# Kernel tuning notes

Hardware: AMD Instinct MI355X
Metric: run time of the kernel (lower is better)

## Reference

```python
import jax, jax.numpy as jnp
import numpy as np

B, FDIM, H, E = 16384, 512, 256, 128  # batch, feature_dim, lstm hidden, scenario encoding


def setup_inputs() -> dict:
    key = jax.random.key(0)
    ks = jax.random.split(key, 24)
    p = lambda k, shape: (jax.random.normal(k, shape, jnp.float32) * 0.05)
    return {
        "base_timeline": jax.random.normal(ks[0], (B, FDIM), jnp.float32),
        "counterfactual_scenario": jax.random.normal(ks[1], (B, FDIM), jnp.float32),
        # scenario_encoder: Linear(512,256) -> ReLU -> Linear(256,128)
        "w_se1": p(ks[2], (256, FDIM)), "b_se1": p(ks[3], (256,)),
        "w_se2": p(ks[4], (E, 256)), "b_se2": p(ks[5], (E,)),
        # LSTM layer 0: input 128, hidden 256 (gate order i,f,g,o)
        "w_ih0": p(ks[6], (4 * H, E)), "w_hh0": p(ks[7], (4 * H, H)),
        "b_ih0": p(ks[8], (4 * H,)), "b_hh0": p(ks[9], (4 * H,)),
        # LSTM layer 1: input 256, hidden 256
        "w_ih1": p(ks[10], (4 * H, H)), "w_hh1": p(ks[11], (4 * H, H)),
        "b_ih1": p(ks[12], (4 * H,)), "b_hh1": p(ks[13], (4 * H,)),
        # outcome_modifier: Linear(384,256) -> ReLU -> Linear(256,512) -> Tanh
        "w_om1": p(ks[14], (256, H + E)), "b_om1": p(ks[15], (256,)),
        "w_om2": p(ks[16], (FDIM, 256)), "b_om2": p(ks[17], (FDIM,)),
        # probability_estimator: Linear(512,128) -> ReLU -> Linear(128,1) -> Sigmoid
        "w_pe1": p(ks[18], (E, FDIM)), "b_pe1": p(ks[19], (E,)),
        "w_pe2": p(ks[20], (1, E)), "b_pe2": p(ks[21], (1,)),
        "num_steps": 10,
    }


def _lstm_cell(x_pre, h, c, w_hh, b_hh):
    gates = x_pre + h @ w_hh.T + b_hh  # [B, 4H]
    i, f, g, o = jnp.split(gates, 4, axis=-1)
    c = jax.nn.sigmoid(f) * c + jax.nn.sigmoid(i) * jnp.tanh(g)
    h = jax.nn.sigmoid(o) * jnp.tanh(c)
    return h, c


def reference(base_timeline, counterfactual_scenario,
              w_se1, b_se1, w_se2, b_se2,
              w_ih0, w_hh0, b_ih0, b_hh0,
              w_ih1, w_hh1, b_ih1, b_hh1,
              w_om1, b_om1, w_om2, b_om2,
              w_pe1, b_pe1, w_pe2, b_pe2,
              num_steps):
    # scenario encoding [B, 128]
    s = jax.nn.relu(counterfactual_scenario @ w_se1.T + b_se1) @ w_se2.T + b_se2
    bsz = base_timeline.shape[0]
    h = w_hh0.shape[1]
    # LSTM layer-0 input is the same scenario encoding each step -> precompute
    x_pre0 = s @ w_ih0.T + b_ih0  # [B, 4H]

    def step(carry, _):
        cur, h0, c0, h1, c1 = carry
        h0, c0 = _lstm_cell(x_pre0, h0, c0, w_hh0, b_hh0)
        x1 = h0 @ w_ih1.T + b_ih1
        h1, c1 = _lstm_cell(x1, h1, c1, w_hh1, b_hh1)
        comb = jnp.concatenate([h1, s], axis=-1)  # [B, 384]
        mod = jnp.tanh(jax.nn.relu(comb @ w_om1.T + b_om1) @ w_om2.T + b_om2)
        nxt = cur + 0.1 * mod
        prob = jax.nn.sigmoid(jax.nn.relu(nxt @ w_pe1.T + b_pe1) @ w_pe2.T + b_pe2)
        return (nxt, h0, c0, h1, c1), (nxt, prob)

    z = jnp.zeros((bsz, h), base_timeline.dtype)
    (final, _, _, _, _), (states, probs) = jax.lax.scan(
        step, (base_timeline, z, z, z, z), None, length=num_steps)
    alternate_timeline = jnp.swapaxes(states, 0, 1)        # [B, num_steps, 512]
    timeline_probabilities = jnp.swapaxes(probs, 0, 1)     # [B, num_steps, 1]
    return alternate_timeline, timeline_probabilities, s, final
```

## Files before the change

### kernel.cpp

```cpp
#include <hip/hip_runtime.h>

typedef short bf16x8 __attribute__((ext_vector_type(8)));
typedef float f32x4 __attribute__((ext_vector_type(4)));

#define DEV __device__ __forceinline__

DEV short f2bf(float f) {
  union { float f; unsigned u; } v; v.f = f;
  unsigned r = v.u + 0x7FFFu + ((v.u >> 16) & 1u);
  return (short)(r >> 16);
}
DEV float bf2f(short s) {
  union { unsigned u; float f; } v; v.u = ((unsigned)(unsigned short)s) << 16;
  return v.f;
}
DEV float sigm(float x) { return 1.0f / (1.0f + __expf(-x)); }
DEV float tanh_(float x) {
  float a = fabsf(x);
  float e = __expf(-2.0f * a);
  float t = (1.0f - e) / (1.0f + e);
  return copysignf(t, x);
}

#define LDS_S    0
#define LDS_H0   16384
#define LDS_H1   49152
#define LDS_U    81920
#define LDS_NX   81920
#define LDS_PROB 147456
#define LDS_CF   16384
#define LDS_SZ   149504

#define OFF_SE1 0
#define OFF_SE2 131072
#define OFF_W0  163840
#define OFF_W1  557056
#define OFF_OM1 1081344
#define OFF_OM2 1179648
#define OFF_PE1 1310720

__global__ void prep_frag(const float* __restrict__ srcA, const float* __restrict__ srcB,
                          short* __restrict__ dst, int N, int K, int ksplit)
{
  const int e = blockIdx.x * 256 + threadIdx.x;
  if (e >= N * K) return;
  const int f = e >> 9;
  const int rix = e & 511;
  const int lane = rix >> 3, j = rix & 7;
  const int KK = K >> 5;
  const int ntile = f / KK, kk = f - ntile * KK;
  const int n = ntile * 16 + (lane & 15);
  const int k = kk * 32 + ((lane >> 4) << 3) + j;
  float v;
  if (k < ksplit) v = srcA[(size_t)n * ksplit + k];
  else            v = srcB[(size_t)n * (K - ksplit) + (k - ksplit)];
  dst[e] = f2bf(v);
}

template<int NT, int MT>
DEV void zacc(f32x4 (&acc)[NT][MT]) {
  #pragma unroll
  for (int n = 0; n < NT; ++n)
    #pragma unroll
    for (int m = 0; m < MT; ++m)
      acc[n][m] = (f32x4){0.f, 0.f, 0.f, 0.f};
}

template<int KK, int NT, int MT>
DEV void mm_tiles(const char* sm, int aBase0, int aStride0, int splitKB,
                  int aBase1, int aStride1,
                  const short* __restrict__ wf, int ntBase, int ntStride,
                  f32x4 (&acc)[NT][MT], int lane)
{
  const int l15 = lane & 15, l4 = lane >> 4;
  const short* wp = wf + lane * 8;
  bf16x8 b[2][NT];
  #pragma unroll
  for (int nt = 0; nt < NT; ++nt)
    b[0][nt] = *(const bf16x8*)(wp + (size_t)((ntBase + nt * ntStride) * KK) * 512);
  #pragma unroll
  for (int kk = 0; kk < KK; ++kk) {
    const int cb = kk & 1, nb = cb ^ 1;
    if (kk + 1 < KK) {
      #pragma unroll
      for (int nt = 0; nt < NT; ++nt)
        b[nb][nt] = *(const bf16x8*)(wp + (size_t)((ntBase + nt * ntStride) * KK + kk + 1) * 512);
    }
    const int kb = kk * 64 + l4 * 16;
    bf16x8 a[MT];
    #pragma unroll
    for (int m = 0; m < MT; ++m) {
      const int r = m * 16 + l15;
      int off;
      if (kb < splitKB) off = aBase0 + r * aStride0 + (kb ^ ((r & 7) << 4));
      else              off = aBase1 + r * aStride1 + ((kb - splitKB) ^ ((r & 7) << 4));
      a[m] = *(const bf16x8*)(sm + off);
    }
    #pragma unroll
    for (int nt = 0; nt < NT; ++nt)
      #pragma unroll
      for (int m = 0; m < MT; ++m)
        acc[nt][m] = __builtin_amdgcn_mfma_f32_16x16x32_bf16(a[m], b[cb][nt], acc[nt][m], 0, 0, 0);
  }
}

DEV void lstm_ew(f32x4 (&acc)[4][4], f32x4 bv, unsigned (&cpk)[8], unsigned (&hp)[16], int hoff)
{
  #pragma unroll
  for (int m = 0; m < 4; ++m)
    #pragma unroll
    for (int qh = 0; qh < 2; ++qh) {
      const int pi = m * 2 + qh;
      const unsigned oldc = cpk[pi];
      unsigned newc = 0, newh = 0;
      #pragma unroll
      for (int ql = 0; ql < 2; ++ql) {
        const int q = qh * 2 + ql;
        const float gi = acc[0][m][q] + bv[0];
        const float gf = acc[1][m][q] + bv[1];
        const float gg = acc[2][m][q] + bv[2];
        const float go = acc[3][m][q] + bv[3];
        const float cold = bf2f((short)((oldc >> (ql * 16)) & 0xFFFFu));
        const float c = sigm(gf) * cold + sigm(gi) * tanh_(gg);
        const float h = sigm(go) * tanh_(c);
        newc |= ((unsigned)(unsigned short)f2bf(c)) << (ql * 16);
        newh |= ((unsigned)(unsigned short)f2bf(h)) << (ql * 16);
      }
      cpk[pi] = newc;
      hp[hoff + pi] = newh;
    }
}

__global__ __launch_bounds__(512, 2) void atg_main(
    const float* __restrict__ base, const float* __restrict__ cf,
    const float* __restrict__ b_se1, const float* __restrict__ b_se2,
    const float* __restrict__ b_ih0, const float* __restrict__ b_hh0,
    const float* __restrict__ b_ih1, const float* __restrict__ b_hh1,
    const float* __restrict__ b_om1, const float* __restrict__ b_om2,
    const float* __restrict__ b_pe1, const float* __restrict__ w_pe2,
    const float* __restrict__ b_pe2,
    const short* __restrict__ wsb,
    float* __restrict__ outStates, float* __restrict__ probs,
    float* __restrict__ outS, float* __restrict__ outFinal, int nsteps)
{
  __shared__ __align__(16) char sm[LDS_SZ];
  const int tid = threadIdx.x;
  const int lane = tid & 63, wid = tid >> 6;
  const int l15 = lane & 15, l4 = lane >> 4;
  const int row0 = blockIdx.x * 64;

  float curv[64];
  #pragma unroll
  for (int nt = 0; nt < 4; ++nt)
    #pragma unroll
    for (int m = 0; m < 4; ++m)
      #pragma unroll
      for (int q = 0; q < 4; ++q)
        curv[nt * 16 + m * 4 + q] =
            base[(size_t)(row0 + m * 16 + l4 * 4 + q) * 512 + wid * 64 + nt * 16 + l15];

  {
    const int r = tid >> 3, ci = tid & 7;
    const float* src = cf + (size_t)(row0 + r) * 512;
    #pragma unroll
    for (int i = 0; i < 16; ++i) {
      const int c = ci * 4 + i * 32;
      const float4 v = *(const float4*)(src + c);
      short4 h; h.x = f2bf(v.x); h.y = f2bf(v.y); h.z = f2bf(v.z); h.w = f2bf(v.w);
      *(short4*)(sm + LDS_CF + r * 1024 + ((c * 2) ^ ((r & 7) << 4))) = h;
    }
  }
  __syncthreads();

  {
    f32x4 acc[2][4]; zacc(acc);
    mm_tiles<16, 2, 4>(sm, LDS_CF, 1024, 1 << 28, LDS_CF, 1024, wsb + OFF_SE1, wid * 2, 1, acc, lane);
    #pragma unroll
    for (int nt = 0; nt < 2; ++nt) {
      const int cc = wid * 32 + nt * 16 + l15;
      const float bv = b_se1[cc];
      #pragma unroll
      for (int m = 0; m < 4; ++m)
        #pragma unroll
        for (int q = 0; q < 4; ++q) {
          const int rr = m * 16 + l4 * 4 + q;
          const float u = fmaxf(acc[nt][m][q] + bv, 0.0f);
          *(short*)(sm + LDS_U + rr * 512 + ((cc * 2) ^ ((rr & 7) << 4))) = f2bf(u);
        }
    }
  }
  __syncthreads();

  {
    f32x4 acc[1][4]; zacc(acc);
    mm_tiles<8, 1, 4>(sm, LDS_U, 512, 1 << 28, LDS_U, 512, wsb + OFF_SE2, wid, 1, acc, lane);
    const int cc = wid * 16 + l15;
    const float bv = b_se2[cc];
    #pragma unroll
    for (int m = 0; m < 4; ++m)
      #pragma unroll
      for (int q = 0; q < 4; ++q) {
        const int rr = m * 16 + l4 * 4 + q;
        const float v = acc[0][m][q] + bv;
        __builtin_nontemporal_store(v, outS + (size_t)(row0 + rr) * 128 + cc);
        *(short*)(sm + LDS_S + rr * 256 + ((cc * 2) ^ ((rr & 7) << 4))) = f2bf(v);
      }
    #pragma unroll
    for (int i = 0; i < 8; ++i)
      *(f32x4*)(sm + LDS_H0 + tid * 128 + i * 16) = (f32x4){0.f, 0.f, 0.f, 0.f};
  }
  __syncthreads();

  f32x4 b0v[2], b1v[2];
  #pragma unroll
  for (int js = 0; js < 2; ++js) {
    f32x4 t0, t1;
    #pragma unroll
    for (int g = 0; g < 4; ++g) {
      const int c = g * 256 + wid * 32 + js * 16 + l15;
      t0[g] = b_ih0[c] + b_hh0[c];
      t1[g] = b_ih1[c] + b_hh1[c];
    }
    b0v[js] = t0; b1v[js] = t1;
  }

  unsigned c0a[8], c0b[8], c1a[8], c1b[8];
  #pragma unroll
  for (int i = 0; i < 8; ++i) { c0a[i] = 0u; c0b[i] = 0u; c1a[i] = 0u; c1b[i] = 0u; }

  for (int step = 0; step < nsteps; ++step) {
    unsigned hp[16];
    {
      f32x4 acc[4][4]; zacc(acc);
      mm_tiles<12, 4, 4>(sm, LDS_S, 256, 256, LDS_H0, 512, wsb + OFF_W0, wid * 2 + 0, 16, acc, lane);
      lstm_ew(acc, b0v[0], c0a, hp, 0);
    }
    {
      f32x4 acc[4][4]; zacc(acc);
      mm_tiles<12, 4, 4>(sm, LDS_S, 256, 256, LDS_H0, 512, wsb + OFF_W0, wid * 2 + 1, 16, acc, lane);
      lstm_ew(acc, b0v[1], c0b, hp, 8);
    }
    __syncthreads();
    #pragma unroll
    for (int js = 0; js < 2; ++js)
      #pragma unroll
      for (int m = 0; m < 4; ++m)
        #pragma unroll
        for (int q = 0; q < 4; ++q) {
          const int rr = m * 16 + l4 * 4 + q;
          const int cc = wid * 32 + js * 16 + l15;
          const unsigned v = hp[js * 8 + m * 2 + (q >> 1)] >> ((q & 1) * 16);
          *(short*)(sm + LDS_H0 + rr * 512 + ((cc * 2) ^ ((rr & 7) << 4))) = (short)v;
        }
    __syncthreads();
    {
      f32x4 acc[4][4]; zacc(acc);
      mm_tiles<16, 4, 4>(sm, LDS_H0, 512, 512, LDS_H1, 512, wsb + OFF_W1, wid * 2 + 0, 16, acc, lane);
      lstm_ew(acc, b1v[0], c1a, hp, 0);
    }
    {
      f32x4 acc[4][4]; zacc(acc);
      mm_tiles<16, 4, 4>(sm, LDS_H0, 512, 512, LDS_H1, 512, wsb + OFF_W1, wid * 2 + 1, 16, acc, lane);
      lstm_ew(acc, b1v[1], c1b, hp, 8);
    }
    __syncthreads();
    #pragma unroll
    for (int js = 0; js < 2; ++js)
      #pragma unroll
      for (int m = 0; m < 4; ++m)
        #pragma unroll
        for (int q = 0; q < 4; ++q) {
          const int rr = m * 16 + l4 * 4 + q;
          const int cc = wid * 32 + js * 16 + l15;
          const unsigned v = hp[js * 8 + m * 2 + (q >> 1)] >> ((q & 1) * 16);
          *(short*)(sm + LDS_H1 + rr * 512 + ((cc * 2) ^ ((rr & 7) << 4))) = (short)v;
        }
    __syncthreads();
    {
      f32x4 acc[2][4]; zacc(acc);
      mm_tiles<12, 2, 4>(sm, LDS_H1, 512, 512, LDS_S, 256, wsb + OFF_OM1, wid * 2, 1, acc, lane);
      float bo1[2];
      #pragma unroll
      for (int nt = 0; nt < 2; ++nt) bo1[nt] = b_om1[wid * 32 + nt * 16 + l15];
      #pragma unroll
      for (int nt = 0; nt < 2; ++nt)
        #pragma unroll
        for (int m = 0; m < 4; ++m)
          #pragma unroll
          for (int q = 0; q < 4; ++q) {
            const int rr = m * 16 + l4 * 4 + q;
            const int cc = wid * 32 + nt * 16 + l15;
            const float u = fmaxf(acc[nt][m][q] + bo1[nt], 0.0f);
            *(short*)(sm + LDS_U + rr * 512 + ((cc * 2) ^ ((rr & 7) << 4))) = f2bf(u);
          }
    }
    __syncthreads();
    {
      float bo2[4];
      #pragma unroll
      for (int nt = 0; nt < 4; ++nt) bo2[nt] = b_om2[wid * 64 + nt * 16 + l15];
      f32x4 acc[4][4]; zacc(acc);
      mm_tiles<8, 4, 4>(sm, LDS_U, 512, 1 << 28, LDS_U, 512, wsb + OFF_OM2, wid * 4, 1, acc, lane);
      #pragma unroll
      for (int nt = 0; nt < 4; ++nt)
        #pragma unroll
        for (int m = 0; m < 4; ++m)
          #pragma unroll
          for (int q = 0; q < 4; ++q) {
            const int rr = m * 16 + l4 * 4 + q;
            const size_t rg = row0 + rr;
            const int cc = wid * 64 + nt * 16 + l15;
            const int ci = nt * 16 + m * 4 + q;
            const float nx = curv[ci] + 0.1f * tanh_(acc[nt][m][q] + bo2[nt]);
            curv[ci] = nx;
            __builtin_nontemporal_store(nx, outStates + (rg * nsteps + step) * 512 + cc);
            if (step == nsteps - 1)
              __builtin_nontemporal_store(nx, outFinal + rg * 512 + cc);
          }
    }
    __syncthreads();
    #pragma unroll
    for (int nt = 0; nt < 4; ++nt)
      #pragma unroll
      for (int m = 0; m < 4; ++m)
        #pragma unroll
        for (int q = 0; q < 4; ++q) {
          const int rr = m * 16 + l4 * 4 + q;
          const int cc = wid * 64 + nt * 16 + l15;
          *(short*)(sm + LDS_NX + rr * 1024 + ((cc * 2) ^ ((rr & 7) << 4))) =
              f2bf(curv[nt * 16 + m * 4 + q]);
        }
    __syncthreads();
    {
      const int cc = wid * 16 + l15;
      const float bp1 = b_pe1[cc];
      const float w2v = w_pe2[cc];
      f32x4 acc[1][4]; zacc(acc);
      mm_tiles<16, 1, 4>(sm, LDS_NX, 1024, 1 << 28, LDS_NX, 1024, wsb + OFF_PE1, wid, 1, acc, lane);
      float part[16];
      #pragma unroll
      for (int m = 0; m < 4; ++m)
        #pragma unroll
        for (int q = 0; q < 4; ++q)
          part[m * 4 + q] = fmaxf(acc[0][m][q] + bp1, 0.0f) * w2v;
      #pragma unroll
      for (int d = 1; d < 16; d <<= 1)
        #pragma unroll
        for (int i = 0; i < 16; ++i)
          part[i] += __shfl_xor(part[i], d);
      if (l15 == 0) {
        #pragma unroll
        for (int m = 0; m < 4; ++m)
          #pragma unroll
          for (int q = 0; q < 4; ++q)
            *(float*)(sm + LDS_PROB + (wid * 64 + m * 16 + l4 * 4 + q) * 4) = part[m * 4 + q];
      }
    }
    __syncthreads();
    if (tid < 64) {
      float ssum = b_pe2[0];
      #pragma unroll
      for (int w = 0; w < 8; ++w)
        ssum += *(const float*)(sm + LDS_PROB + (w * 64 + tid) * 4);
      const float p = 1.0f / (1.0f + __expf(-ssum));
      __builtin_nontemporal_store(p, probs + (size_t)(row0 + tid) * nsteps + step);
    }
  }
}

extern "C" void kernel_launch(void* const* d_in, const int* in_sizes, int n_in,
                              void* d_out, int out_size, void* d_ws, size_t ws_size,
                              hipStream_t stream)
{
  const float* base  = (const float*)d_in[0];
  const float* cf    = (const float*)d_in[1];
  const float* w_se1 = (const float*)d_in[2];
  const float* b_se1 = (const float*)d_in[3];
  const float* w_se2 = (const float*)d_in[4];
  const float* b_se2 = (const float*)d_in[5];
  const float* w_ih0 = (const float*)d_in[6];
  const float* w_hh0 = (const float*)d_in[7];
  const float* b_ih0 = (const float*)d_in[8];
  const float* b_hh0 = (const float*)d_in[9];
  const float* w_ih1 = (const float*)d_in[10];
  const float* w_hh1 = (const float*)d_in[11];
  const float* b_ih1 = (const float*)d_in[12];
  const float* b_hh1 = (const float*)d_in[13];
  const float* w_om1 = (const float*)d_in[14];
  const float* b_om1 = (const float*)d_in[15];
  const float* w_om2 = (const float*)d_in[16];
  const float* b_om2 = (const float*)d_in[17];
  const float* w_pe1 = (const float*)d_in[18];
  const float* b_pe1 = (const float*)d_in[19];
  const float* w_pe2 = (const float*)d_in[20];
  const float* b_pe2 = (const float*)d_in[21];

  const int B = in_sizes[0] / 512;
  const long nsteps = ((long)out_size - (long)B * 640) / ((long)B * 513);
  short* wsb = (short*)d_ws;
  float* out = (float*)d_out;

  auto prep = [&](const float* A, const float* Bp, long off, int N, int K, int ks) {
    const int total = N * K;
    prep_frag<<<dim3((total + 255) / 256), dim3(256), 0, stream>>>(A, Bp, wsb + off, N, K, ks);
  };
  prep(w_se1, w_se1, OFF_SE1, 256, 512, 512);
  prep(w_se2, w_se2, OFF_SE2, 128, 256, 256);
  prep(w_ih0, w_hh0, OFF_W0, 1024, 384, 128);
  prep(w_ih1, w_hh1, OFF_W1, 1024, 512, 256);
  prep(w_om1, w_om1, OFF_OM1, 256, 384, 384);
  prep(w_om2, w_om2, OFF_OM2, 512, 256, 256);
  prep(w_pe1, w_pe1, OFF_PE1, 128, 512, 512);

  float* probs = out + (size_t)B * nsteps * 512;
  float* outS  = out + (size_t)B * nsteps * 513;
  float* outF  = outS + (size_t)B * 128;
  atg_main<<<dim3(B / 64), dim3(512), 0, stream>>>(base, cf, b_se1, b_se2, b_ih0, b_hh0,
      b_ih1, b_hh1, b_om1, b_om2, b_pe1, w_pe2, b_pe2, wsb, out, probs, outS, outF, (int)nsteps);
}
```

Baseline: 3.341 ms.

## Double block to 16 waves, halve per-wave tiles, add ring-buffered weight prefetch

```diff
diff --git a/kernel.cpp b/kernel.cpp
--- a/kernel.cpp
+++ b/kernel.cpp
@@ -25,10 +25,8 @@
 #define LDS_S    0
 #define LDS_H0   16384
 #define LDS_H1   49152
-#define LDS_U    81920
-#define LDS_NX   81920
+#define LDS_SLAB 81920
 #define LDS_PROB 147456
-#define LDS_CF   16384
 #define LDS_SZ   149504
 
 #define OFF_SE1 0
@@ -74,18 +72,16 @@
 {
   const int l15 = lane & 15, l4 = lane >> 4;
   const short* wp = wf + lane * 8;
-  bf16x8 b[2][NT];
-  #pragma unroll
-  for (int nt = 0; nt < NT; ++nt)
-    b[0][nt] = *(const bf16x8*)(wp + (size_t)((ntBase + nt * ntStride) * KK) * 512);
+  constexpr int TOT = KK * NT;
+  constexpr int D = TOT < 8 ? TOT : 8;
+  bf16x8 rb[D];
+  #pragma unroll
+  for (int f = 0; f < D; ++f) {
+    const int kkf = f / NT, ntf = f % NT;
+    rb[f] = *(const bf16x8*)(wp + (size_t)((ntBase + ntf * ntStride) * KK + kkf) * 512);
+  }
   #pragma unroll
   for (int kk = 0; kk < KK; ++kk) {
-    const int cb = kk & 1, nb = cb ^ 1;
-    if (kk + 1 < KK) {
-      #pragma unroll
-      for (int nt = 0; nt < NT; ++nt)
-        b[nb][nt] = *(const bf16x8*)(wp + (size_t)((ntBase + nt * ntStride) * KK + kk + 1) * 512);
-    }
     const int kb = kk * 64 + l4 * 16;
     bf16x8 a[MT];
     #pragma unroll
@@ -97,14 +93,21 @@
       a[m] = *(const bf16x8*)(sm + off);
     }
     #pragma unroll
-    for (int nt = 0; nt < NT; ++nt)
+    for (int nt = 0; nt < NT; ++nt) {
+      const int f = kk * NT + nt;
+      const int slot = f % D;
       #pragma unroll
       for (int m = 0; m < MT; ++m)
-        acc[nt][m] = __builtin_amdgcn_mfma_f32_16x16x32_bf16(a[m], b[cb][nt], acc[nt][m], 0, 0, 0);
-  }
-}
-
-DEV void lstm_ew(f32x4 (&acc)[4][4], f32x4 bv, unsigned (&cpk)[8], unsigned (&hp)[16], int hoff)
+        acc[nt][m] = __builtin_amdgcn_mfma_f32_16x16x32_bf16(a[m], rb[slot], acc[nt][m], 0, 0, 0);
+      if (f + D < TOT) {
+        const int f2 = f + D, kk2 = f2 / NT, nt2 = f2 % NT;
+        rb[slot] = *(const bf16x8*)(wp + (size_t)((ntBase + nt2 * ntStride) * KK + kk2) * 512);
+      }
+    }
+  }
+}
+
+DEV void lstm_ew(f32x4 (&acc)[4][4], f32x4 bv, unsigned (&cpk)[8], unsigned (&hp)[8])
 {
   #pragma unroll
   for (int m = 0; m < 4; ++m)
@@ -127,11 +130,11 @@
         newh |= ((unsigned)(unsigned short)f2bf(h)) << (ql * 16);
       }
       cpk[pi] = newc;
-      hp[hoff + pi] = newh;
-    }
-}
-
-__global__ __launch_bounds__(512, 2) void atg_main(
+      hp[pi] = newh;
+    }
+}
+
+__global__ __launch_bounds__(1024, 4) void atg_main(
     const float* __restrict__ base, const float* __restrict__ cf,
     const float* __restrict__ b_se1, const float* __restrict__ b_se2,
     const float* __restrict__ b_ih0, const float* __restrict__ b_hh0,
@@ -149,51 +152,48 @@
   const int l15 = lane & 15, l4 = lane >> 4;
   const int row0 = blockIdx.x * 64;
 
-  float curv[64];
-  #pragma unroll
-  for (int nt = 0; nt < 4; ++nt)
+  float curv[32];
+  #pragma unroll
+  for (int i = 0; i < 2; ++i)
     #pragma unroll
     for (int m = 0; m < 4; ++m)
       #pragma unroll
       for (int q = 0; q < 4; ++q)
-        curv[nt * 16 + m * 4 + q] =
-            base[(size_t)(row0 + m * 16 + l4 * 4 + q) * 512 + wid * 64 + nt * 16 + l15];
+        curv[i * 16 + m * 4 + q] =
+            base[(size_t)(row0 + m * 16 + l4 * 4 + q) * 512 + (wid * 2 + i) * 16 + l15];
 
   {
-    const int r = tid >> 3, ci = tid & 7;
+    const int r = tid >> 4, ci = tid & 15;
     const float* src = cf + (size_t)(row0 + r) * 512;
     #pragma unroll
-    for (int i = 0; i < 16; ++i) {
-      const int c = ci * 4 + i * 32;
+    for (int i = 0; i < 8; ++i) {
+      const int c = ci * 4 + i * 64;
       const float4 v = *(const float4*)(src + c);
       short4 h; h.x = f2bf(v.x); h.y = f2bf(v.y); h.z = f2bf(v.z); h.w = f2bf(v.w);
-      *(short4*)(sm + LDS_CF + r * 1024 + ((c * 2) ^ ((r & 7) << 4))) = h;
-    }
-  }
-  __syncthreads();
-
-  {
-    f32x4 acc[2][4]; zacc(acc);
-    mm_tiles<16, 2, 4>(sm, LDS_CF, 1024, 1 << 28, LDS_CF, 1024, wsb + OFF_SE1, wid * 2, 1, acc, lane);
-    #pragma unroll
-    for (int nt = 0; nt < 2; ++nt) {
-      const int cc = wid * 32 + nt * 16 + l15;
-      const float bv = b_se1[cc];
-      #pragma unroll
-      for (int m = 0; m < 4; ++m)
-        #pragma unroll
-        for (int q = 0; q < 4; ++q) {
-          const int rr = m * 16 + l4 * 4 + q;
-          const float u = fmaxf(acc[nt][m][q] + bv, 0.0f);
-          *(short*)(sm + LDS_U + rr * 512 + ((cc * 2) ^ ((rr & 7) << 4))) = f2bf(u);
-        }
+      *(short4*)(sm + LDS_SLAB + r * 1024 + ((c * 2) ^ ((r & 7) << 4))) = h;
     }
   }
   __syncthreads();
 
   {
     f32x4 acc[1][4]; zacc(acc);
-    mm_tiles<8, 1, 4>(sm, LDS_U, 512, 1 << 28, LDS_U, 512, wsb + OFF_SE2, wid, 1, acc, lane);
+    mm_tiles<16, 1, 4>(sm, LDS_SLAB, 1024, 1 << 28, LDS_SLAB, 1024, wsb + OFF_SE1, wid, 1, acc, lane);
+    const int cc = wid * 16 + l15;
+    const float bv = b_se1[cc];
+    #pragma unroll
+    for (int m = 0; m < 4; ++m)
+      #pragma unroll
+      for (int q = 0; q < 4; ++q) {
+        const int rr = m * 16 + l4 * 4 + q;
+        const float u = fmaxf(acc[0][m][q] + bv, 0.0f);
+        *(short*)(sm + LDS_H0 + rr * 512 + ((cc * 2) ^ ((rr & 7) << 4))) = f2bf(u);
+      }
+  }
+  __syncthreads();
+
+  if (wid < 8) {
+    f32x4 acc[1][4]; zacc(acc);
+    mm_tiles<8, 1, 4>(sm, LDS_H0, 512, 1 << 28, LDS_H0, 512, wsb + OFF_SE2, wid, 1, acc, lane);
     const int cc = wid * 16 + l15;
     const float bv = b_se2[cc];
     #pragma unroll
@@ -205,138 +205,114 @@
         __builtin_nontemporal_store(v, outS + (size_t)(row0 + rr) * 128 + cc);
         *(short*)(sm + LDS_S + rr * 256 + ((cc * 2) ^ ((rr & 7) << 4))) = f2bf(v);
       }
-    #pragma unroll
-    for (int i = 0; i < 8; ++i)
-      *(f32x4*)(sm + LDS_H0 + tid * 128 + i * 16) = (f32x4){0.f, 0.f, 0.f, 0.f};
   }
   __syncthreads();
-
-  f32x4 b0v[2], b1v[2];
-  #pragma unroll
-  for (int js = 0; js < 2; ++js) {
-    f32x4 t0, t1;
-    #pragma unroll
-    for (int g = 0; g < 4; ++g) {
-      const int c = g * 256 + wid * 32 + js * 16 + l15;
-      t0[g] = b_ih0[c] + b_hh0[c];
-      t1[g] = b_ih1[c] + b_hh1[c];
-    }
-    b0v[js] = t0; b1v[js] = t1;
-  }
-
-  unsigned c0a[8], c0b[8], c1a[8], c1b[8];
-  #pragma unroll
-  for (int i = 0; i < 8; ++i) { c0a[i] = 0u; c0b[i] = 0u; c1a[i] = 0u; c1b[i] = 0u; }
+  #pragma unroll
+  for (int i = 0; i < 4; ++i)
+    *(f32x4*)(sm + LDS_H0 + tid * 64 + i * 16) = (f32x4){0.f, 0.f, 0.f, 0.f};
+  __syncthreads();
+
+  f32x4 b0v, b1v;
+  #pragma unroll
+  for (int g = 0; g < 4; ++g) {
+    const int c = g * 256 + wid * 16 + l15;
+    b0v[g] = b_ih0[c] + b_hh0[c];
+    b1v[g] = b_ih1[c] + b_hh1[c];
+  }
+  const float bo1 = b_om1[wid * 16 + l15];
+  float bo2[2];
+  #pragma unroll
+  for (int i = 0; i < 2; ++i) bo2[i] = b_om2[(wid * 2 + i) * 16 + l15];
+  float bp1 = 0.f, w2v = 0.f;
+  if (wid < 8) { bp1 = b_pe1[wid * 16 + l15]; w2v = w_pe2[wid * 16 + l15]; }
+
+  unsigned c0[8], c1[8];
+  #pragma unroll
+  for (int i = 0; i < 8; ++i) { c0[i] = 0u; c1[i] = 0u; }
 
   for (int step = 0; step < nsteps; ++step) {
-    unsigned hp[16];
+    unsigned hp[8];
     {
       f32x4 acc[4][4]; zacc(acc);
-      mm_tiles<12, 4, 4>(sm, LDS_S, 256, 256, LDS_H0, 512, wsb + OFF_W0, wid * 2 + 0, 16, acc, lane);
-      lstm_ew(acc, b0v[0], c0a, hp, 0);
-    }
+      mm_tiles<12, 4, 4>(sm, LDS_S, 256, 256, LDS_H0, 512, wsb + OFF_W0, wid, 16, acc, lane);
+      lstm_ew(acc, b0v, c0, hp);
+    }
+    __syncthreads();
+    #pragma unroll
+    for (int m = 0; m < 4; ++m)
+      #pragma unroll
+      for (int q = 0; q < 4; ++q) {
+        const int rr = m * 16 + l4 * 4 + q;
+        const int cc = wid * 16 + l15;
+        const unsigned v = hp[m * 2 + (q >> 1)] >> ((q & 1) * 16);
+        *(short*)(sm + LDS_H0 + rr * 512 + ((cc * 2) ^ ((rr & 7) << 4))) = (short)v;
+      }
+    __syncthreads();
     {
       f32x4 acc[4][4]; zacc(acc);
-      mm_tiles<12, 4, 4>(sm, LDS_S, 256, 256, LDS_H0, 512, wsb + OFF_W0, wid * 2 + 1, 16, acc, lane);
-      lstm_ew(acc, b0v[1], c0b, hp, 8);
-    }
-    __syncthreads();
-    #pragma unroll
-    for (int js = 0; js < 2; ++js)
+      mm_tiles<16, 4, 4>(sm, LDS_H0, 512, 512, LDS_H1, 512, wsb + OFF_W1, wid, 16, acc, lane);
+      lstm_ew(acc, b1v, c1, hp);
+    }
+    __syncthreads();
+    #pragma unroll
+    for (int m = 0; m < 4; ++m)
+      #pragma unroll
+      for (int q = 0; q < 4; ++q) {
+        const int rr = m * 16 + l4 * 4 + q;
+        const int cc = wid * 16 + l15;
+        const unsigned v = hp[m * 2 + (q >> 1)] >> ((q & 1) * 16);
+        *(short*)(sm + LDS_H1 + rr * 512 + ((cc * 2) ^ ((rr & 7) << 4))) = (short)v;
+      }
+    __syncthreads();
+    {
+      f32x4 acc[1][4]; zacc(acc);
+      mm_tiles<12, 1, 4>(sm, LDS_H1, 512, 512, LDS_S, 256, wsb + OFF_OM1, wid, 1, acc, lane);
+      const int cc = wid * 16 + l15;
       #pragma unroll
       for (int m = 0; m < 4; ++m)
         #pragma unroll
         for (int q = 0; q < 4; ++q) {
           const int rr = m * 16 + l4 * 4 + q;
-          const int cc = wid * 32 + js * 16 + l15;
-          const unsigned v = hp[js * 8 + m * 2 + (q >> 1)] >> ((q & 1) * 16);
-          *(short*)(sm + LDS_H0 + rr * 512 + ((cc * 2) ^ ((rr & 7) << 4))) = (short)v;
+          const float u = fmaxf(acc[0][m][q] + bo1, 0.0f);
+          *(short*)(sm + LDS_SLAB + rr * 512 + ((cc * 2) ^ ((rr & 7) << 4))) = f2bf(u);
         }
-    __syncthreads();
-    {
-      f32x4 acc[4][4]; zacc(acc);
-      mm_tiles<16, 4, 4>(sm, LDS_H0, 512, 512, LDS_H1, 512, wsb + OFF_W1, wid * 2 + 0, 16, acc, lane);
-      lstm_ew(acc, b1v[0], c1a, hp, 0);
-    }
-    {
-      f32x4 acc[4][4]; zacc(acc);
-      mm_tiles<16, 4, 4>(sm, LDS_H0, 512, 512, LDS_H1, 512, wsb + OFF_W1, wid * 2 + 1, 16, acc, lane);
-      lstm_ew(acc, b1v[1], c1b, hp, 8);
-    }
-    __syncthreads();
-    #pragma unroll
-    for (int js = 0; js < 2; ++js)
-      #pragma unroll
-      for (int m = 0; m < 4; ++m)
-        #pragma unroll
-        for (int q = 0; q < 4; ++q) {
-          const int rr = m * 16 + l4 * 4 + q;
-          const int cc = wid * 32 + js * 16 + l15;
-          const unsigned v = hp[js * 8 + m * 2 + (q >> 1)] >> ((q & 1) * 16);
-          *(short*)(sm + LDS_H1 + rr * 512 + ((cc * 2) ^ ((rr & 7) << 4))) = (short)v;
-        }
+    }
     __syncthreads();
     {
       f32x4 acc[2][4]; zacc(acc);
-      mm_tiles<12, 2, 4>(sm, LDS_H1, 512, 512, LDS_S, 256, wsb + OFF_OM1, wid * 2, 1, acc, lane);
-      float bo1[2];
-      #pragma unroll
-      for (int nt = 0; nt < 2; ++nt) bo1[nt] = b_om1[wid * 32 + nt * 16 + l15];
-      #pragma unroll
-      for (int nt = 0; nt < 2; ++nt)
+      mm_tiles<8, 2, 4>(sm, LDS_SLAB, 512, 1 << 28, LDS_SLAB, 512, wsb + OFF_OM2, wid * 2, 1, acc, lane);
+      #pragma unroll
+      for (int i = 0; i < 2; ++i) {
+        const int cc = (wid * 2 + i) * 16 + l15;
         #pragma unroll
         for (int m = 0; m < 4; ++m)
           #pragma unroll
           for (int q = 0; q < 4; ++q) {
             const int rr = m * 16 + l4 * 4 + q;
-            const int cc = wid * 32 + nt * 16 + l15;
-            const float u = fmaxf(acc[nt][m][q] + bo1[nt], 0.0f);
-            *(short*)(sm + LDS_U + rr * 512 + ((cc * 2) ^ ((rr & 7) << 4))) = f2bf(u);
+            const int ci = i * 16 + m * 4 + q;
+            const float nx = curv[ci] + 0.1f * tanh_(acc[i][m][q] + bo2[i]);
+            curv[ci] = nx;
+            __builtin_nontemporal_store(nx,
+                outStates + ((size_t)(row0 + rr) * nsteps + step) * 512 + cc);
           }
-    }
-    __syncthreads();
-    {
-      float bo2[4];
-      #pragma unroll
-      for (int nt = 0; nt < 4; ++nt) bo2[nt] = b_om2[wid * 64 + nt * 16 + l15];
-      f32x4 acc[4][4]; zacc(acc);
-      mm_tiles<8, 4, 4>(sm, LDS_U, 512, 1 << 28, LDS_U, 512, wsb + OFF_OM2, wid * 4, 1, acc, lane);
-      #pragma unroll
-      for (int nt = 0; nt < 4; ++nt)
-        #pragma unroll
-        for (int m = 0; m < 4; ++m)
-          #pragma unroll
-          for (int q = 0; q < 4; ++q) {
-            const int rr = m * 16 + l4 * 4 + q;
-            const size_t rg = row0 + rr;
-            const int cc = wid * 64 + nt * 16 + l15;
-            const int ci = nt * 16 + m * 4 + q;
-            const float nx = curv[ci] + 0.1f * tanh_(acc[nt][m][q] + bo2[nt]);
-            curv[ci] = nx;
-            __builtin_nontemporal_store(nx, outStates + (rg * nsteps + step) * 512 + cc);
-            if (step == nsteps - 1)
-              __builtin_nontemporal_store(nx, outFinal + rg * 512 + cc);
-          }
-    }
-    __syncthreads();
-    #pragma unroll
-    for (int nt = 0; nt < 4; ++nt)
+      }
+    }
+    __syncthreads();
+    #pragma unroll
+    for (int i = 0; i < 2; ++i)
       #pragma unroll
       for (int m = 0; m < 4; ++m)
         #pragma unroll
         for (int q = 0; q < 4; ++q) {
           const int rr = m * 16 + l4 * 4 + q;
-          const int cc = wid * 64 + nt * 16 + l15;
-          *(short*)(sm + LDS_NX + rr * 1024 + ((cc * 2) ^ ((rr & 7) << 4))) =
-              f2bf(curv[nt * 16 + m * 4 + q]);
+          const int cc = (wid * 2 + i) * 16 + l15;
+          *(short*)(sm + LDS_SLAB + rr * 1024 + ((cc * 2) ^ ((rr & 7) << 4))) =
+              f2bf(curv[i * 16 + m * 4 + q]);
         }
     __syncthreads();
-    {
-      const int cc = wid * 16 + l15;
-      const float bp1 = b_pe1[cc];
-      const float w2v = w_pe2[cc];
+    if (wid < 8) {
       f32x4 acc[1][4]; zacc(acc);
-      mm_tiles<16, 1, 4>(sm, LDS_NX, 1024, 1 << 28, LDS_NX, 1024, wsb + OFF_PE1, wid, 1, acc, lane);
+      mm_tiles<16, 1, 4>(sm, LDS_SLAB, 1024, 1 << 28, LDS_SLAB, 1024, wsb + OFF_PE1, wid, 1, acc, lane);
       float part[16];
       #pragma unroll
       for (int m = 0; m < 4; ++m)
@@ -366,6 +342,15 @@
       __builtin_nontemporal_store(p, probs + (size_t)(row0 + tid) * nsteps + step);
     }
   }
+
+  #pragma unroll
+  for (int i = 0; i < 2; ++i)
+    #pragma unroll
+    for (int m = 0; m < 4; ++m)
+      #pragma unroll
+      for (int q = 0; q < 4; ++q)
+        __builtin_nontemporal_store(curv[i * 16 + m * 4 + q],
+            outFinal + (size_t)(row0 + m * 16 + l4 * 4 + q) * 512 + (wid * 2 + i) * 16 + l15);
 }
 
 extern "C" void kernel_launch(void* const* d_in, const int* in_sizes, int n_in,
@@ -415,6 +400,6 @@
   float* probs = out + (size_t)B * nsteps * 512;
   float* outS  = out + (size_t)B * nsteps * 513;
   float* outF  = outS + (size_t)B * 128;
-  atg_main<<<dim3(B / 64), dim3(512), 0, stream>>>(base, cf, b_se1, b_se2, b_ih0, b_hh0,
+  atg_main<<<dim3(B / 64), dim3(1024), 0, stream>>>(base, cf, b_se1, b_se2, b_ih0, b_hh0,
       b_ih1, b_hh1, b_om1, b_om2, b_pe1, w_pe2, b_pe2, wsb, out, probs, outS, outF, (int)nsteps);
 }
```

Result: faster. 3.105 ms (-7.0%).
